# Kernel tuning notes

Measured on AMD Instinct MI355X. Metric: run time of the kernel, lower is better.

The kernel has to match this reference:

```python
import jax, jax.numpy as jnp
import numpy as np


def setup_inputs() -> dict:
    key = jax.random.key(0)
    k1, k2, k3 = jax.random.split(key, 3)
    B, S, Q, K, D = 64, 512, 800, 4, 64
    q_data = jax.random.normal(k1, (B, S, Q), dtype=jnp.float32)
    r_data = jax.random.randint(k2, (B, S), 0, K)
    # learned params (xavier-ish scale)
    Wq = jax.random.normal(k3, (D, Q), dtype=jnp.float32) * (0.5 * (2.0 / (Q + D)) ** 0.5)
    bq = jnp.zeros((D,), dtype=jnp.float32)
    Wr = jax.random.normal(jax.random.fold_in(key, 7), (1, K), dtype=jnp.float32) * (0.5 * (2.0 / (K + 1)) ** 0.5)
    br = jnp.zeros((1,), dtype=jnp.float32)
    return {"q_data": q_data, "r_data": r_data, "Wq": Wq, "bq": bq,
            "Wr": Wr, "br": br, "n_questions": Q, "n_cats": K}


def reference(q_data, r_data, Wq, bq, Wr, br, n_questions, n_cats):
    # Vectorized over (batch, seq): original looped over t in python.
    K = n_cats
    k_idx = jnp.arange(K, dtype=q_data.dtype)                      # [K]
    dist = jnp.abs(k_idx[None, None, :] - r_data[..., None].astype(q_data.dtype)) / (K - 1)  # [B,S,K]
    weights = jnp.maximum(1.0 - dist, 0.0)                        # [B,S,K]
    # response_weights: Linear(K -> 1) then sigmoid -> scalar gate per (b,s)
    gate = jax.nn.sigmoid(jnp.einsum('bsk,ok->bso', weights, Wr) + br)  # [B,S,1]
    weighted_q = q_data * gate                                    # [B,S,Q]
    # question_embed: Linear(Q -> D)
    out = jnp.einsum('bsq,dq->bsd', weighted_q, Wq) + bq          # [B,S,D]
    return out
```

## Files before the change

kernel.cpp:

```cpp
#include <hip/hip_runtime.h>
#include <hip/hip_bf16.h>
#include <stdint.h>


#define QD 800
#define DD 64
#define M_TOTAL 32768
#define KT 25
#define PIPE 3

typedef __attribute__((ext_vector_type(8))) short bf16x8;
typedef __attribute__((ext_vector_type(4))) float f32x4;

typedef const __attribute__((address_space(1))) uint32_t* gas1_u32;
typedef __attribute__((address_space(3))) uint32_t* las3_u32;

static __device__ __forceinline__ void gll16(const void* g, const void* l) {
  __builtin_amdgcn_global_load_lds((gas1_u32)(uintptr_t)g,
                                   (las3_u32)(uint32_t)(uintptr_t)l, 16, 0, 0);
}

static __device__ __forceinline__ short f2bf(float f) {
  union { __hip_bfloat16 h; short s; } u;
  u.h = __float2bfloat16(f);
  return u.s;
}

static __device__ __forceinline__ bf16x8 pack8(f32x4 lo, f32x4 hi) {
  bf16x8 r;
  r[0] = f2bf(lo.x); r[1] = f2bf(lo.y); r[2] = f2bf(lo.z); r[3] = f2bf(lo.w);
  r[4] = f2bf(hi.x); r[5] = f2bf(hi.y); r[6] = f2bf(hi.z); r[7] = f2bf(hi.w);
  return r;
}

static __device__ __forceinline__ bf16x8 load_split8(const float* __restrict__ p) {
  return pack8(*reinterpret_cast<const f32x4*>(p),
               *reinterpret_cast<const f32x4*>(p + 16));
}

__global__ void convert_wq_kernel(const float* __restrict__ Wq, short* __restrict__ Bb) {
  int idx = blockIdx.x * 256 + threadIdx.x;
  int kt = idx >> 8;
  int acc = (idx >> 6) & 3;
  int lane = idx & 63;
  int l15 = lane & 15, lhi = lane >> 4;
  const float* p = Wq + (acc * 16 + l15) * QD + kt * 32 + lhi * 4;
  *reinterpret_cast<bf16x8*>(Bb + (size_t)idx * 8) = load_split8(p);
}

static __device__ __forceinline__ void stage(
    const float* __restrict__ qbase, const short* __restrict__ blob, int kt,
    float* bufA, short* bufB, int t, int wave) {
  const float* qk = qbase + kt * 32;
  const short* bk = blob + (size_t)kt * 2048;
#pragma unroll
  for (int j = 0; j < 2; ++j) {
    int s = j * 128 + t;
    int row = s >> 3;
    int kseg = (s & 7) ^ (row & 7);
    gll16(qk + (size_t)row * QD + kseg * 4, bufA + (j * 128 + wave * 64) * 4);
  }
#pragma unroll
  for (int j = 0; j < 2; ++j) {
    int s = j * 128 + t;
    gll16(bk + s * 8, bufB + (j * 128 + wave * 64) * 8);
  }
}

__global__ __launch_bounds__(128, 2) void sold_kernel(
    const float* __restrict__ q, const int* __restrict__ rdat,
    const short* __restrict__ Bb, const float* __restrict__ bq,
    const float* __restrict__ Wr, const float* __restrict__ br,
    float* __restrict__ out) {
  const int t = threadIdx.x;
  const int lane = t & 63;
  const int wave = t >> 6;
  const int l15 = lane & 15;
  const int lhi = lane >> 4;
  const int m0 = blockIdx.x * 32;

  __shared__ __align__(16) float bufA[PIPE][1024];
  __shared__ __align__(16) short bufB[PIPE][2048];

  const float* qbase = q + (size_t)m0 * QD;

  f32x4 acc0 = {0.f, 0.f, 0.f, 0.f};
  f32x4 acc1 = {0.f, 0.f, 0.f, 0.f};
  f32x4 acc2 = {0.f, 0.f, 0.f, 0.f};
  f32x4 acc3 = {0.f, 0.f, 0.f, 0.f};

  stage(qbase, Bb, 0, bufA[0], bufB[0], t, wave);
  stage(qbase, Bb, 1, bufA[1], bufB[1], t, wave);

  const int row32 = wave * 16 + l15;
  const int rb = row32 & 7;
  const int offA_lo = row32 * 32 + ((0 + lhi) ^ rb) * 4;
  const int offA_hi = row32 * 32 + ((4 + lhi) ^ rb) * 4;

  for (int kt = 0; kt < KT; ++kt) {
    __syncthreads();
    int nx = kt + 2;
    int sl = kt % PIPE;
    if (nx < KT) stage(qbase, Bb, nx, bufA[nx % PIPE], bufB[nx % PIPE], t, wave);

    const float* A = bufA[sl];
    const short* B = bufB[sl];
    f32x4 alo = *reinterpret_cast<const f32x4*>(A + offA_lo);
    f32x4 ahi = *reinterpret_cast<const f32x4*>(A + offA_hi);
    bf16x8 a = pack8(alo, ahi);
    bf16x8 b0 = *reinterpret_cast<const bf16x8*>(B + (0 * 64 + lane) * 8);
    bf16x8 b1 = *reinterpret_cast<const bf16x8*>(B + (1 * 64 + lane) * 8);
    bf16x8 b2 = *reinterpret_cast<const bf16x8*>(B + (2 * 64 + lane) * 8);
    bf16x8 b3 = *reinterpret_cast<const bf16x8*>(B + (3 * 64 + lane) * 8);
    acc0 = __builtin_amdgcn_mfma_f32_16x16x32_bf16(a, b0, acc0, 0, 0, 0);
    acc1 = __builtin_amdgcn_mfma_f32_16x16x32_bf16(a, b1, acc1, 0, 0, 0);
    acc2 = __builtin_amdgcn_mfma_f32_16x16x32_bf16(a, b2, acc2, 0, 0, 0);
    acc3 = __builtin_amdgcn_mfma_f32_16x16x32_bf16(a, b3, acc3, 0, 0, 0);
  }

  float wr[4] = {Wr[0], Wr[1], Wr[2], Wr[3]};
  float brv = br[0];
  float lut[4];
  const float inv3 = 1.0f / 3.0f;
#pragma unroll
  for (int r = 0; r < 4; ++r) {
    float s = brv;
#pragma unroll
    for (int k = 0; k < 4; ++k) {
      float w = fmaxf(1.0f - fabsf((float)(k - r)) * inv3, 0.0f);
      s += w * wr[k];
    }
    lut[r] = 1.0f / (1.0f + __expf(-s));
  }

  float bqv0 = bq[0 * 16 + l15];
  float bqv1 = bq[1 * 16 + l15];
  float bqv2 = bq[2 * 16 + l15];
  float bqv3 = bq[3 * 16 + l15];

#pragma unroll
  for (int r = 0; r < 4; ++r) {
    int row = m0 + wave * 16 + lhi * 4 + r;
    float g = lut[rdat[row]];
    float* orow = out + (size_t)row * DD + l15;
    orow[0]  = acc0[r] * g + bqv0;
    orow[16] = acc1[r] * g + bqv1;
    orow[32] = acc2[r] * g + bqv2;
    orow[48] = acc3[r] * g + bqv3;
  }
}

__global__ __launch_bounds__(256, 2) void sold_direct(
    const float* __restrict__ q, const int* __restrict__ rdat,
    const float* __restrict__ Wq, const float* __restrict__ bq,
    const float* __restrict__ Wr, const float* __restrict__ br,
    float* __restrict__ out) {
  const int lane = threadIdx.x & 63;
  const int wave = threadIdx.x >> 6;
  const int l15 = lane & 15;
  const int lhi = lane >> 4;
  const int m0 = blockIdx.x * 64 + wave * 16;
  const float* aptr = q + (size_t)(m0 + l15) * QD + lhi * 4;
  const float* w0 = Wq + (0 * 16 + l15) * QD + lhi * 4;
  const float* w1 = Wq + (1 * 16 + l15) * QD + lhi * 4;
  const float* w2 = Wq + (2 * 16 + l15) * QD + lhi * 4;
  const float* w3 = Wq + (3 * 16 + l15) * QD + lhi * 4;
  f32x4 acc0 = {0.f,0.f,0.f,0.f}, acc1 = {0.f,0.f,0.f,0.f};
  f32x4 acc2 = {0.f,0.f,0.f,0.f}, acc3 = {0.f,0.f,0.f,0.f};
#pragma unroll 5
  for (int kt = 0; kt < KT; ++kt) {
    bf16x8 a  = load_split8(aptr + kt * 32);
    bf16x8 b0 = load_split8(w0 + kt * 32);
    bf16x8 b1 = load_split8(w1 + kt * 32);
    bf16x8 b2 = load_split8(w2 + kt * 32);
    bf16x8 b3 = load_split8(w3 + kt * 32);
    acc0 = __builtin_amdgcn_mfma_f32_16x16x32_bf16(a, b0, acc0, 0, 0, 0);
    acc1 = __builtin_amdgcn_mfma_f32_16x16x32_bf16(a, b1, acc1, 0, 0, 0);
    acc2 = __builtin_amdgcn_mfma_f32_16x16x32_bf16(a, b2, acc2, 0, 0, 0);
    acc3 = __builtin_amdgcn_mfma_f32_16x16x32_bf16(a, b3, acc3, 0, 0, 0);
  }
  float wr[4] = {Wr[0], Wr[1], Wr[2], Wr[3]};
  float brv = br[0], lut[4];
  const float inv3 = 1.0f / 3.0f;
#pragma unroll
  for (int r = 0; r < 4; ++r) {
    float s = brv;
#pragma unroll
    for (int k = 0; k < 4; ++k)
      s += fmaxf(1.0f - fabsf((float)(k - r)) * inv3, 0.0f) * wr[k];
    lut[r] = 1.0f / (1.0f + __expf(-s));
  }
  float bqv0 = bq[l15], bqv1 = bq[16 + l15], bqv2 = bq[32 + l15], bqv3 = bq[48 + l15];
#pragma unroll
  for (int r = 0; r < 4; ++r) {
    int row = m0 + lhi * 4 + r;
    float g = lut[rdat[row]];
    float* orow = out + (size_t)row * DD + l15;
    orow[0]  = acc0[r] * g + bqv0;
    orow[16] = acc1[r] * g + bqv1;
    orow[32] = acc2[r] * g + bqv2;
    orow[48] = acc3[r] * g + bqv3;
  }
}

extern "C" void kernel_launch(void* const* d_in, const int* in_sizes, int n_in,
                              void* d_out, int out_size, void* d_ws, size_t ws_size,
                              hipStream_t stream) {
  const float* q    = (const float*)d_in[0];
  const int*   rdat = (const int*)d_in[1];
  const float* Wq   = (const float*)d_in[2];
  const float* bq   = (const float*)d_in[3];
  const float* Wr   = (const float*)d_in[4];
  const float* br   = (const float*)d_in[5];
  float* out = (float*)d_out;

  const size_t need_ws = (size_t)KT * 2048 * sizeof(short);
  if (ws_size >= need_ws) {
    short* Bb = (short*)d_ws;
    convert_wq_kernel<<<KT, 256, 0, stream>>>(Wq, Bb);
    sold_kernel<<<M_TOTAL / 32, 128, 0, stream>>>(q, rdat, Bb, bq, Wr, br, out);
  } else {
    sold_direct<<<M_TOTAL / 64, 256, 0, stream>>>(q, rdat, Wq, bq, Wr, br, out);
  }
}
```

Before: 171.3 us.

## Replace LDS staging with register-prefetch pipeline of depth five

Drops the shared-memory double/triple buffering built on global_load_lds and __syncthreads. Each wave now loads its A rows and pre-converted B fragments straight from global memory into registers, with five k-steps kept in flight. The loop is fully unrolled and separated by sched_barriers. Blocks grow to 256 threads covering 64 rows. This removes LDS round-trips and block-wide barriers, but costs many more VGPRs (five stages of A and B fragments), which may limit occupancy. Each wave also re-reads B from global or L2 on its own instead of sharing it through LDS.

New measurement: 169.8 us. No clear change (-0.9%).

```diff
diff --git a/kernel.cpp b/kernel.cpp
--- a/kernel.cpp
+++ b/kernel.cpp
@@ -1,24 +1,15 @@
 #include <hip/hip_runtime.h>
 #include <hip/hip_bf16.h>
-#include <stdint.h>
 
 
 #define QD 800
 #define DD 64
 #define M_TOTAL 32768
 #define KT 25
-#define PIPE 3
+#define DEPTH 5
 
 typedef __attribute__((ext_vector_type(8))) short bf16x8;
 typedef __attribute__((ext_vector_type(4))) float f32x4;
-
-typedef const __attribute__((address_space(1))) uint32_t* gas1_u32;
-typedef __attribute__((address_space(3))) uint32_t* las3_u32;
-
-static __device__ __forceinline__ void gll16(const void* g, const void* l) {
-  __builtin_amdgcn_global_load_lds((gas1_u32)(uintptr_t)g,
-                                   (las3_u32)(uint32_t)(uintptr_t)l, 16, 0, 0);
-}
 
 static __device__ __forceinline__ short f2bf(float f) {
   union { __hip_bfloat16 h; short s; } u;
@@ -48,74 +39,60 @@
   *reinterpret_cast<bf16x8*>(Bb + (size_t)idx * 8) = load_split8(p);
 }
 
-static __device__ __forceinline__ void stage(
-    const float* __restrict__ qbase, const short* __restrict__ blob, int kt,
-    float* bufA, short* bufB, int t, int wave) {
-  const float* qk = qbase + kt * 32;
-  const short* bk = blob + (size_t)kt * 2048;
-#pragma unroll
-  for (int j = 0; j < 2; ++j) {
-    int s = j * 128 + t;
-    int row = s >> 3;
-    int kseg = (s & 7) ^ (row & 7);
-    gll16(qk + (size_t)row * QD + kseg * 4, bufA + (j * 128 + wave * 64) * 4);
-  }
-#pragma unroll
-  for (int j = 0; j < 2; ++j) {
-    int s = j * 128 + t;
-    gll16(bk + s * 8, bufB + (j * 128 + wave * 64) * 8);
-  }
-}
-
-__global__ __launch_bounds__(128, 2) void sold_kernel(
+__global__ __launch_bounds__(256, 2) void sold_kernel(
     const float* __restrict__ q, const int* __restrict__ rdat,
     const short* __restrict__ Bb, const float* __restrict__ bq,
     const float* __restrict__ Wr, const float* __restrict__ br,
     float* __restrict__ out) {
-  const int t = threadIdx.x;
-  const int lane = t & 63;
-  const int wave = t >> 6;
+  const int lane = threadIdx.x & 63;
+  const int wave = threadIdx.x >> 6;
   const int l15 = lane & 15;
   const int lhi = lane >> 4;
-  const int m0 = blockIdx.x * 32;
-
-  __shared__ __align__(16) float bufA[PIPE][1024];
-  __shared__ __align__(16) short bufB[PIPE][2048];
-
-  const float* qbase = q + (size_t)m0 * QD;
+  const int m0 = blockIdx.x * 64 + wave * 16;
+
+  const float* ap = q + (size_t)(m0 + l15) * QD + lhi * 4;
+  const short* bp = Bb + (size_t)lane * 8;
+
+  f32x4 aLo[DEPTH], aHi[DEPTH];
+  bf16x8 bfr[DEPTH][4];
+
+#pragma unroll
+  for (int s = 0; s < DEPTH; ++s) {
+    const float* a = ap + s * 32;
+    aLo[s] = *reinterpret_cast<const f32x4*>(a);
+    aHi[s] = *reinterpret_cast<const f32x4*>(a + 16);
+    const short* p = bp + s * 2048;
+    bfr[s][0] = *reinterpret_cast<const bf16x8*>(p + 0 * 512);
+    bfr[s][1] = *reinterpret_cast<const bf16x8*>(p + 1 * 512);
+    bfr[s][2] = *reinterpret_cast<const bf16x8*>(p + 2 * 512);
+    bfr[s][3] = *reinterpret_cast<const bf16x8*>(p + 3 * 512);
+  }
 
   f32x4 acc0 = {0.f, 0.f, 0.f, 0.f};
   f32x4 acc1 = {0.f, 0.f, 0.f, 0.f};
   f32x4 acc2 = {0.f, 0.f, 0.f, 0.f};
   f32x4 acc3 = {0.f, 0.f, 0.f, 0.f};
 
-  stage(qbase, Bb, 0, bufA[0], bufB[0], t, wave);
-  stage(qbase, Bb, 1, bufA[1], bufB[1], t, wave);
-
-  const int row32 = wave * 16 + l15;
-  const int rb = row32 & 7;
-  const int offA_lo = row32 * 32 + ((0 + lhi) ^ rb) * 4;
-  const int offA_hi = row32 * 32 + ((4 + lhi) ^ rb) * 4;
-
+#pragma unroll
   for (int kt = 0; kt < KT; ++kt) {
-    __syncthreads();
-    int nx = kt + 2;
-    int sl = kt % PIPE;
-    if (nx < KT) stage(qbase, Bb, nx, bufA[nx % PIPE], bufB[nx % PIPE], t, wave);
-
-    const float* A = bufA[sl];
-    const short* B = bufB[sl];
-    f32x4 alo = *reinterpret_cast<const f32x4*>(A + offA_lo);
-    f32x4 ahi = *reinterpret_cast<const f32x4*>(A + offA_hi);
-    bf16x8 a = pack8(alo, ahi);
-    bf16x8 b0 = *reinterpret_cast<const bf16x8*>(B + (0 * 64 + lane) * 8);
-    bf16x8 b1 = *reinterpret_cast<const bf16x8*>(B + (1 * 64 + lane) * 8);
-    bf16x8 b2 = *reinterpret_cast<const bf16x8*>(B + (2 * 64 + lane) * 8);
-    bf16x8 b3 = *reinterpret_cast<const bf16x8*>(B + (3 * 64 + lane) * 8);
-    acc0 = __builtin_amdgcn_mfma_f32_16x16x32_bf16(a, b0, acc0, 0, 0, 0);
-    acc1 = __builtin_amdgcn_mfma_f32_16x16x32_bf16(a, b1, acc1, 0, 0, 0);
-    acc2 = __builtin_amdgcn_mfma_f32_16x16x32_bf16(a, b2, acc2, 0, 0, 0);
-    acc3 = __builtin_amdgcn_mfma_f32_16x16x32_bf16(a, b3, acc3, 0, 0, 0);
+    const int s = kt % DEPTH;
+    bf16x8 a = pack8(aLo[s], aHi[s]);
+    acc0 = __builtin_amdgcn_mfma_f32_16x16x32_bf16(a, bfr[s][0], acc0, 0, 0, 0);
+    acc1 = __builtin_amdgcn_mfma_f32_16x16x32_bf16(a, bfr[s][1], acc1, 0, 0, 0);
+    acc2 = __builtin_amdgcn_mfma_f32_16x16x32_bf16(a, bfr[s][2], acc2, 0, 0, 0);
+    acc3 = __builtin_amdgcn_mfma_f32_16x16x32_bf16(a, bfr[s][3], acc3, 0, 0, 0);
+    const int nx = kt + DEPTH;
+    if (nx < KT) {
+      const float* a2 = ap + nx * 32;
+      aLo[s] = *reinterpret_cast<const f32x4*>(a2);
+      aHi[s] = *reinterpret_cast<const f32x4*>(a2 + 16);
+      const short* p = bp + nx * 2048;
+      bfr[s][0] = *reinterpret_cast<const bf16x8*>(p + 0 * 512);
+      bfr[s][1] = *reinterpret_cast<const bf16x8*>(p + 1 * 512);
+      bfr[s][2] = *reinterpret_cast<const bf16x8*>(p + 2 * 512);
+      bfr[s][3] = *reinterpret_cast<const bf16x8*>(p + 3 * 512);
+    }
+    __builtin_amdgcn_sched_barrier(0);
   }
 
   float wr[4] = {Wr[0], Wr[1], Wr[2], Wr[3]};
@@ -140,7 +117,7 @@
 
 #pragma unroll
   for (int r = 0; r < 4; ++r) {
-    int row = m0 + wave * 16 + lhi * 4 + r;
+    int row = m0 + lhi * 4 + r;
     float g = lut[rdat[row]];
     float* orow = out + (size_t)row * DD + l15;
     orow[0]  = acc0[r] * g + bqv0;
@@ -218,7 +195,7 @@
   if (ws_size >= need_ws) {
     short* Bb = (short*)d_ws;
     convert_wq_kernel<<<KT, 256, 0, stream>>>(Wq, Bb);
-    sold_kernel<<<M_TOTAL / 32, 128, 0, stream>>>(q, rdat, Bb, bq, Wr, br, out);
+    sold_kernel<<<M_TOTAL / 64, 256, 0, stream>>>(q, rdat, Bb, bq, Wr, br, out);
   } else {
     sold_direct<<<M_TOTAL / 64, 256, 0, stream>>>(q, rdat, Wq, bq, Wr, br, out);
   }
```
